# Kernel optimization log

Hardware: AMD Instinct MI355X
Metric: run time of the kernel (lower is better)

Reference implementation:

```python
import jax, jax.numpy as jnp
import numpy as np

B, L, D = 8, 1024, 768          # batch, seq_len, d_model
DI, DS, NL, DC = 1536, 16, 2, 4  # d_inner=2*d_model, d_state, n_layers, d_conv
DECAY, INSCALE = 0.9, 0.1
LN_EPS = 1e-5


def setup_inputs() -> dict:
    key = jax.random.key(0)
    ks = jax.random.split(key, 8)
    return {
        "x": jax.random.normal(ks[0], (B, L, D), jnp.float32),
        "in_proj_w": jax.random.normal(ks[1], (NL, D, 2 * DI), jnp.float32) * 0.02,
        "conv_w": jax.random.normal(ks[2], (NL, DI, DC), jnp.float32) * 0.1,
        "conv_b": jnp.zeros((NL, DI), jnp.float32),
        "out_proj_w": jax.random.normal(ks[3], (NL, DI, D), jnp.float32) * 0.02,
        "ln_gamma": jnp.ones((D,), jnp.float32),
        "ln_beta": jnp.zeros((D,), jnp.float32),
        # per-layer, per-timestep random state matrices (torch.randn inside the scan loop)
        "A": jax.random.normal(ks[4], (NL, L, DI, DS), jnp.float32),
        "Bm": jax.random.normal(ks[5], (NL, L, DS, DI), jnp.float32),
    }


def _silu(v):
    return v * jax.nn.sigmoid(v)


def _causal_dwconv(x, w, b):
    # x: [B, L, DI], w: [DI, DC], b: [DI]; torch Conv1d(groups=DI, padding=DC-1)[..., :L]
    xp = jnp.pad(x, ((0, 0), (DC - 1, 0), (0, 0)))
    out = b
    for k in range(DC):  # tiny fixed kernel loop
        out = out + w[:, k] * xp[:, k:k + L, :]
    return out


def _mamba_block(x, Wi, cw, cb, Wo, A_l, B_l):
    xz = jnp.einsum('bld,de->ble', x, Wi)
    x_in, z = jnp.split(xz, 2, axis=-1)          # each [B, L, DI]
    xc = _silu(_causal_dwconv(x_in, cw, cb))
    # selective scan: h_t = 0.9*h_{t-1} + 0.1 * x_t @ A_t ; y_t = h_t @ B_t
    u = INSCALE * jnp.einsum('blc,lcs->bls', xc, A_l)   # [B, L, DS]
    def step(h, u_t):
        h = DECAY * h + u_t
        return h, h
    _, hs = jax.lax.scan(step, jnp.zeros((x.shape[0], DS), x.dtype),
                         jnp.swapaxes(u, 0, 1))          # hs: [L, B, DS]
    x_ssm = jnp.einsum('lbs,lsc->blc', hs, B_l)          # [B, L, DI]
    y = x_ssm * _silu(z)
    return jnp.einsum('blc,cd->bld', y, Wo)


def reference(x, in_proj_w, conv_w, conv_b, out_proj_w, ln_gamma, ln_beta, A, Bm):
    for i in range(NL):  # residual fallback path of MambaSSM
        x = x + _mamba_block(x, in_proj_w[i], conv_w[i], conv_b[i],
                             out_proj_w[i], A[i], Bm[i])
    mu = jnp.mean(x, axis=-1, keepdims=True)
    var = jnp.mean(jnp.square(x - mu), axis=-1, keepdims=True)
    return (x - mu) / jnp.sqrt(var + LN_EPS) * ln_gamma + ln_beta
```

## Files before the change

kernel.cpp:

```cpp
#include <hip/hip_runtime.h>
#include <cstddef>
#include <cstdint>

constexpr int B  = 8;
constexpr int L  = 1024;
constexpr int D  = 768;
constexpr int DI = 1536;
constexpr int DS = 16;
constexpr int NL = 2;
constexpr float DECAY   = 0.9f;
constexpr float INSCALE = 0.1f;
constexpr float LN_EPS  = 1e-5f;

typedef __attribute__((ext_vector_type(8))) short bf16x8;
typedef __attribute__((ext_vector_type(4))) float f32x4;

typedef __attribute__((address_space(3))) uint32_t       lds_u32;
typedef const __attribute__((address_space(1))) uint32_t glb_u32;

__device__ __forceinline__ float siluf(float v) { return v / (1.0f + expf(-v)); }

__device__ __forceinline__ short f2bf(float f) {
  uint32_t u = __float_as_uint(f);
  u += 0x7fff + ((u >> 16) & 1);
  return (short)(u >> 16);
}
__device__ __forceinline__ float bf2f(short s) {
  return __uint_as_float(((uint32_t)(uint16_t)s) << 16);
}

__device__ __forceinline__ void load_lds16(const short* g, short* l) {
  __builtin_amdgcn_global_load_lds((glb_u32*)g, (lds_u32*)l, 16, 0, 0);
}

__device__ __forceinline__ int xcd_chunked(int lin, int nwg) {
  return (lin & 7) * (nwg >> 3) + (lin >> 3);
}

__global__ __launch_bounds__(256) void prep_kernel(const float* __restrict__ x,
                                                   float* __restrict__ xf,
                                                   short* __restrict__ xb,
                                                   const float* __restrict__ Wi,
                                                   const float* __restrict__ Wo,
                                                   short* __restrict__ Wt_i,
                                                   short* __restrict__ Wt_o) {
  int bid = blockIdx.x;
  if (bid < 6144) {
    int i = bid * 256 + threadIdx.x;
    float4 v = ((const float4*)x)[i];
    ((float4*)xf)[i] = v;
    short4 s;
    s.x = f2bf(v.x); s.y = f2bf(v.y); s.z = f2bf(v.z); s.w = f2bf(v.w);
    ((short4*)xb)[i] = s;
    return;
  }
  bid -= 6144;
  __shared__ float t[32][33];
  const int layer = bid / 3456;
  bid %= 3456;
  const float* W; short* Wt; int K, N, bx, by;
  if (bid < 2304) {
    W  = Wi  + (size_t)layer * D * 2 * DI;
    Wt = Wt_i + (size_t)layer * 2 * DI * D;
    K = D; N = 2 * DI; bx = bid % 96; by = bid / 96;
  } else {
    bid -= 2304;
    W  = Wo  + (size_t)layer * DI * D;
    Wt = Wt_o + (size_t)layer * D * DI;
    K = DI; N = D; bx = bid % 24; by = bid / 24;
  }
  const int n0 = bx * 32, k0 = by * 32;
  const int tx = threadIdx.x & 31, ty = threadIdx.x >> 5;
#pragma unroll
  for (int r = ty; r < 32; r += 8) t[r][tx] = W[(size_t)(k0 + r) * N + n0 + tx];
  __syncthreads();
#pragma unroll
  for (int r = ty; r < 32; r += 8) Wt[(size_t)(n0 + r) * K + k0 + tx] = f2bf(t[tx][r]);
}

template<int MODE>
__global__ __launch_bounds__(256) void gemm_bt(const short* __restrict__ A,
                                               const short* __restrict__ Bt,
                                               float* __restrict__ Pf,
                                               short* __restrict__ Pb,
                                               int M, int N, int K) {
  __shared__ short As[3][128 * 32];
  __shared__ short Bs[3][128 * 32];
  const int tid  = threadIdx.x;
  const int lane = tid & 63;
  const int w    = tid >> 6;
  const int wm   = w >> 1;
  const int wn   = w & 1;

  const int gx   = gridDim.x;
  const int lin  = blockIdx.y * gx + blockIdx.x;
  const int lgc  = xcd_chunked(lin, gx * gridDim.y);
  const int bn   = (lgc % gx) * 128;
  const int bm   = (lgc / gx) * 128;

  const int seg0 = w * 2;
  const int lane16 = lane << 4;
  const int P0 = (seg0 << 10) + lane16;
  const int Q0 = P0 ^ (((P0 >> 7) & 3) << 4);
  const int row0 = Q0 >> 6;
  const int g0   = (Q0 >> 4) & 3;
  const int P1 = ((seg0 + 1) << 10) + lane16;
  const int Q1 = P1 ^ (((P1 >> 7) & 3) << 4);
  const int row1 = Q1 >> 6;
  const int g1   = (Q1 >> 4) & 3;

  const short* gA0 = A  + (size_t)(bm + row0) * K + g0 * 8;
  const short* gA1 = A  + (size_t)(bm + row1) * K + g1 * 8;
  const short* gB0 = Bt + (size_t)(bn + row0) * K + g0 * 8;
  const short* gB1 = Bt + (size_t)(bn + row1) * K + g1 * 8;

  f32x4 acc[4][4];
#pragma unroll
  for (int i = 0; i < 4; ++i)
#pragma unroll
    for (int j = 0; j < 4; ++j) acc[i][j] = (f32x4)(0.f);

  const int fr = lane & 15;
  const int h8 = (lane >> 4) << 3;
  const int NT = K / 32;

  auto stage = [&](int bi, int k0) {
    load_lds16(gA0 + k0, &As[bi][(size_t)seg0 * 512]);
    load_lds16(gA1 + k0, &As[bi][(size_t)(seg0 + 1) * 512]);
    load_lds16(gB0 + k0, &Bs[bi][(size_t)seg0 * 512]);
    load_lds16(gB1 + k0, &Bs[bi][(size_t)(seg0 + 1) * 512]);
  };
  auto compute = [&](int bi) {
    bf16x8 af[4], bfr[4];
#pragma unroll
    for (int i = 0; i < 4; ++i) {
      const int r = wm * 64 + i * 16 + fr;
      int si = (r << 5) + h8;
      si ^= ((r >> 1) & 3) << 3;
      af[i] = *(const bf16x8*)&As[bi][si];
    }
#pragma unroll
    for (int j = 0; j < 4; ++j) {
      const int r = wn * 64 + j * 16 + fr;
      int si = (r << 5) + h8;
      si ^= ((r >> 1) & 3) << 3;
      bfr[j] = *(const bf16x8*)&Bs[bi][si];
    }
#pragma unroll
    for (int i = 0; i < 4; ++i)
#pragma unroll
      for (int j = 0; j < 4; ++j)
        acc[i][j] = __builtin_amdgcn_mfma_f32_16x16x32_bf16(af[i], bfr[j], acc[i][j], 0, 0, 0);
  };

  stage(0, 0);
  stage(1, 32);
  asm volatile("s_waitcnt vmcnt(4)" ::: "memory");
  asm volatile("s_barrier" ::: "memory");

  for (int t = 0; t < NT; t += 3) {
#pragma unroll
    for (int q = 0; q < 3; ++q) {
      const int tt = t + q;
      if (tt + 2 < NT) stage((q + 2) % 3, (tt + 2) * 32);
      compute(q);
      if (tt + 1 < NT) {
        if (tt + 2 < NT) asm volatile("s_waitcnt vmcnt(4)" ::: "memory");
        else             asm volatile("s_waitcnt vmcnt(0)" ::: "memory");
        asm volatile("s_barrier" ::: "memory");
      }
    }
  }

  const int orow = (lane >> 4) * 4;
  const int ocol = lane & 15;
#pragma unroll
  for (int i = 0; i < 4; ++i) {
#pragma unroll
    for (int r = 0; r < 4; ++r) {
      const size_t row = (size_t)(bm + wm * 64 + i * 16 + orow + r);
#pragma unroll
      for (int j = 0; j < 4; ++j) {
        const int col = bn + wn * 64 + j * 16 + ocol;
        float v = acc[i][j][r];
        if (MODE == 0) {
          if (col < DI) Pb[row * DI + col] = f2bf(v);
          else          Pb[(size_t)M * DI + row * DI + col - DI] = f2bf(v);
        } else {
          float o = Pf[row * N + col] + v;
          Pf[row * N + col] = o;
          Pb[row * N + col] = f2bf(o);
        }
      }
    }
  }
}

constexpr int CSL = DI / 4;
__global__ __launch_bounds__(256) void conv_u_kernel(const short* __restrict__ xin,
                                                     const float* __restrict__ cw,
                                                     const float* __restrict__ cb,
                                                     const float* __restrict__ A_l,
                                                     float* __restrict__ u_part) {
  const int lgc = xcd_chunked(blockIdx.x, L * 4);
  const int p = lgc & 3;
  const int l = lgc >> 2;
  const int c_base = p * CSL;
  __shared__ float xs[B][CSL];
  __shared__ float part[4][4][32];

  for (int i = threadIdx.x; i < B * (CSL / 4); i += 256) {
    const int b  = i / (CSL / 4);
    const int c4 = (i % (CSL / 4)) * 4;
    const int c  = c_base + c4;
    float4 q0 = *(const float4*)&cw[(c + 0) * 4];
    float4 q1 = *(const float4*)&cw[(c + 1) * 4];
    float4 q2 = *(const float4*)&cw[(c + 2) * 4];
    float4 q3 = *(const float4*)&cw[(c + 3) * 4];
    float4 acc = *(const float4*)&cb[c];
    const short* xp = xin + (size_t)b * L * DI + c;
#pragma unroll
    for (int k = 0; k < 4; ++k) {
      int lk = l - 3 + k;
      if (lk >= 0) {
        short4 xv = *(const short4*)&xp[(size_t)lk * DI];
        acc.x += (&q0.x)[k] * bf2f(xv.x);
        acc.y += (&q1.x)[k] * bf2f(xv.y);
        acc.z += (&q2.x)[k] * bf2f(xv.z);
        acc.w += (&q3.x)[k] * bf2f(xv.w);
      }
    }
    acc.x = siluf(acc.x); acc.y = siluf(acc.y);
    acc.z = siluf(acc.z); acc.w = siluf(acc.w);
    *(float4*)&xs[b][c4] = acc;
  }
  __syncthreads();

  const int s4 = threadIdx.x & 3;
  const int cg = threadIdx.x >> 2;
  const float* Ap = A_l + (size_t)l * DI * DS + s4 * 4;

  float4 acc[B];
#pragma unroll
  for (int b = 0; b < B; ++b) acc[b] = make_float4(0.f, 0.f, 0.f, 0.f);

#pragma unroll
  for (int c0 = 0; c0 < CSL; c0 += 64) {
    const int cl = c0 + cg;
    float4 a4 = *(const float4*)&Ap[(size_t)(c_base + cl) * DS];
#pragma unroll
    for (int b = 0; b < B; ++b) {
      float xv = xs[b][cl];
      acc[b].x += xv * a4.x; acc[b].y += xv * a4.y;
      acc[b].z += xv * a4.z; acc[b].w += xv * a4.w;
    }
  }

#pragma unroll
  for (int off = 32; off >= 4; off >>= 1) {
#pragma unroll
    for (int b = 0; b < B; ++b) {
      acc[b].x += __shfl_down(acc[b].x, off, 64);
      acc[b].y += __shfl_down(acc[b].y, off, 64);
      acc[b].z += __shfl_down(acc[b].z, off, 64);
      acc[b].w += __shfl_down(acc[b].w, off, 64);
    }
  }
  const int wv = threadIdx.x >> 6, lane = threadIdx.x & 63;
  if (lane < 4) {
#pragma unroll
    for (int b = 0; b < B; ++b) {
      part[wv][lane][b * 4 + 0] = acc[b].x;
      part[wv][lane][b * 4 + 1] = acc[b].y;
      part[wv][lane][b * 4 + 2] = acc[b].z;
      part[wv][lane][b * 4 + 3] = acc[b].w;
    }
  }
  __syncthreads();
  if (threadIdx.x < 128) {
    const int o  = threadIdx.x;
    const int b  = o >> 4;
    const int ss = (o >> 2) & 3;
    const int jj = o & 3;
    float s = part[0][ss][b * 4 + jj] + part[1][ss][b * 4 + jj] +
              part[2][ss][b * 4 + jj] + part[3][ss][b * 4 + jj];
    u_part[((size_t)l * 4 + p) * 128 + o] = INSCALE * s;
  }
}

__global__ __launch_bounds__(256) void scan_kernel(const float* __restrict__ u_part,
                                                   float* __restrict__ hs) {
  const int t = blockIdx.x;
  const int i = threadIdx.x;
  __shared__ float csc[256];

  float v[4];
#pragma unroll
  for (int j = 0; j < 4; ++j) {
    const float* up = u_part + ((size_t)(4 * i + j) * 4) * 128 + t;
    v[j] = (up[0] + up[128]) + (up[256] + up[384]);
  }
  const float p0 = v[0];
  const float p1 = p0 * DECAY + v[1];
  const float p2 = p1 * DECAY + v[2];
  const float p3 = p2 * DECAY + v[3];

  csc[i] = p3;
  __syncthreads();
  float f = DECAY * DECAY * DECAY * DECAY;
  for (int d = 1; d < 256; d <<= 1) {
    float add = (i >= d) ? csc[i - d] : 0.f;
    __syncthreads();
    csc[i] += add * f;
    __syncthreads();
    f *= f;
  }
  const float H = (i > 0) ? csc[i - 1] : 0.f;

  const float a1 = DECAY, a2 = DECAY * DECAY, a3 = a2 * DECAY, a4 = a2 * a2;
  float* hp = hs + (size_t)(4 * i) * 128 + t;
  hp[0]   = p0 + H * a1;
  hp[128] = p1 + H * a2;
  hp[256] = p2 + H * a3;
  hp[384] = p3 + H * a4;
}

__global__ __launch_bounds__(256) void xssm_kernel(const float* __restrict__ hs,
                                                   const float* __restrict__ B_l,
                                                   const short* __restrict__ zb,
                                                   short* __restrict__ y) {
  const int l0 = blockIdx.x * 2;
  const int cb = blockIdx.y * (DI / 3);
  __shared__ float hsl[2][128];
  const int t = threadIdx.x;
  hsl[t >> 7][t & 127] = hs[(size_t)(l0 + (t >> 7)) * 128 + (t & 127)];
  __syncthreads();

  const int li = t >> 7;
  const int l  = l0 + li;
  const int c  = cb + (t & 127) * 4;
  const float* Bp = B_l + (size_t)l * DS * DI + c;

  float4 acc[B];
#pragma unroll
  for (int b = 0; b < B; ++b) acc[b] = make_float4(0.f, 0.f, 0.f, 0.f);
#pragma unroll
  for (int s = 0; s < DS; ++s) {
    float4 bv = *(const float4*)&Bp[(size_t)s * DI];
#pragma unroll
    for (int b = 0; b < B; ++b) {
      float hv = hsl[li][b * DS + s];
      acc[b].x += hv * bv.x; acc[b].y += hv * bv.y;
      acc[b].z += hv * bv.z; acc[b].w += hv * bv.w;
    }
  }
#pragma unroll
  for (int b = 0; b < B; ++b) {
    short4 zs = *(const short4*)&zb[((size_t)b * L + l) * DI + c];
    short4 o;
    o.x = f2bf(acc[b].x * siluf(bf2f(zs.x)));
    o.y = f2bf(acc[b].y * siluf(bf2f(zs.y)));
    o.z = f2bf(acc[b].z * siluf(bf2f(zs.z)));
    o.w = f2bf(acc[b].w * siluf(bf2f(zs.w)));
    *(short4*)&y[((size_t)b * L + l) * DI + c] = o;
  }
}

__global__ __launch_bounds__(256) void ln_kernel(const float* __restrict__ x,
                                                 const float* __restrict__ gam,
                                                 const float* __restrict__ bet,
                                                 float* __restrict__ out) {
  const int row = blockIdx.x;
  const int t = threadIdx.x;
  const float* xr = x + (size_t)row * D;
  float v0 = xr[t], v1 = xr[t + 256], v2 = xr[t + 512];
  float s = v0 + v1 + v2;
  __shared__ float red[4], red2[4];
  const int wid = t >> 6, lane = t & 63;
#pragma unroll
  for (int off = 32; off > 0; off >>= 1) s += __shfl_down(s, off, 64);
  if (lane == 0) red[wid] = s;
  __syncthreads();
  float mu = (red[0] + red[1] + red[2] + red[3]) * (1.0f / D);
  float d0 = v0 - mu, d1 = v1 - mu, d2 = v2 - mu;
  float q = d0 * d0 + d1 * d1 + d2 * d2;
#pragma unroll
  for (int off = 32; off > 0; off >>= 1) q += __shfl_down(q, off, 64);
  if (lane == 0) red2[wid] = q;
  __syncthreads();
  float var = (red2[0] + red2[1] + red2[2] + red2[3]) * (1.0f / D);
  float rstd = rsqrtf(var + LN_EPS);
  size_t base = (size_t)row * D;
  out[base + t]       = d0 * rstd * gam[t]       + bet[t];
  out[base + t + 256] = d1 * rstd * gam[t + 256] + bet[t + 256];
  out[base + t + 512] = d2 * rstd * gam[t + 512] + bet[t + 512];
}

extern "C" void kernel_launch(void* const* d_in, const int* in_sizes, int n_in,
                              void* d_out, int out_size, void* d_ws, size_t ws_size,
                              hipStream_t stream) {
  (void)in_sizes; (void)n_in; (void)out_size; (void)ws_size;
  const float* x   = (const float*)d_in[0];
  const float* Wi  = (const float*)d_in[1];
  const float* cw  = (const float*)d_in[2];
  const float* cb  = (const float*)d_in[3];
  const float* Wo  = (const float*)d_in[4];
  const float* gam = (const float*)d_in[5];
  const float* bet = (const float*)d_in[6];
  const float* Am  = (const float*)d_in[7];
  const float* Bm  = (const float*)d_in[8];
  float* out = (float*)d_out;

  const size_t MN = (size_t)B * L;

  float* buf_x  = (float*)d_ws;
  short* buf_xb = (short*)(buf_x + MN * D);
  short* xin_b  = buf_xb + MN * D;
  short* zb     = xin_b + MN * DI;
  short* y_bf   = zb + MN * DI;
  float* u_part = (float*)(y_bf + MN * DI);
  float* buf_hs = u_part + (size_t)L * 4 * 128;
  short* Wt_i   = (short*)(buf_hs + (size_t)L * 128);
  short* Wt_o   = Wt_i + (size_t)NL * 2 * DI * D;

  prep_kernel<<<6144 + 3456 * NL, 256, 0, stream>>>(x, buf_x, buf_xb, Wi, Wo, Wt_i, Wt_o);

  for (int layer = 0; layer < NL; ++layer) {
    const float* cw_l = cw + (size_t)layer * DI * 4;
    const float* cb_l = cb + (size_t)layer * DI;
    const float* A_l  = Am + (size_t)layer * L * DI * DS;
    const float* B_l  = Bm + (size_t)layer * L * DS * DI;
    const short* Wti_l = Wt_i + (size_t)layer * 2 * DI * D;
    const short* Wto_l = Wt_o + (size_t)layer * D * DI;

    gemm_bt<0><<<dim3(2 * DI / 128, MN / 128), 256, 0, stream>>>(
        buf_xb, Wti_l, nullptr, xin_b, (int)MN, 2 * DI, D);

    conv_u_kernel<<<L * 4, 256, 0, stream>>>(xin_b, cw_l, cb_l, A_l, u_part);

    scan_kernel<<<128, 256, 0, stream>>>(u_part, buf_hs);

    xssm_kernel<<<dim3(L / 2, 3), 256, 0, stream>>>(buf_hs, B_l, zb, y_bf);

    gemm_bt<1><<<dim3(D / 128, MN / 128), 256, 0, stream>>>(
        y_bf, Wto_l, buf_x, buf_xb, (int)MN, D, DI);
  }

  ln_kernel<<<(int)MN, 256, 0, stream>>>(buf_x, gam, bet, out);
}
```

Baseline: 479.3 us.

## Split GEMM into specialized kernels with 64x128 out-proj tile, drop XCD remap

```diff
diff --git a/kernel.cpp b/kernel.cpp
--- a/kernel.cpp
+++ b/kernel.cpp
@@ -31,10 +31,6 @@
 
 __device__ __forceinline__ void load_lds16(const short* g, short* l) {
   __builtin_amdgcn_global_load_lds((glb_u32*)g, (lds_u32*)l, 16, 0, 0);
-}
-
-__device__ __forceinline__ int xcd_chunked(int lin, int nwg) {
-  return (lin & 7) * (nwg >> 3) + (lin >> 3);
 }
 
 __global__ __launch_bounds__(256) void prep_kernel(const float* __restrict__ x,
@@ -78,12 +74,10 @@
   for (int r = ty; r < 32; r += 8) Wt[(size_t)(n0 + r) * K + k0 + tx] = f2bf(t[tx][r]);
 }
 
-template<int MODE>
-__global__ __launch_bounds__(256) void gemm_bt(const short* __restrict__ A,
-                                               const short* __restrict__ Bt,
-                                               float* __restrict__ Pf,
-                                               short* __restrict__ Pb,
-                                               int M, int N, int K) {
+__global__ __launch_bounds__(256) void gemm_bt0(const short* __restrict__ A,
+                                                const short* __restrict__ Bt,
+                                                short* __restrict__ Pb,
+                                                int M, int N, int K) {
   __shared__ short As[3][128 * 32];
   __shared__ short Bs[3][128 * 32];
   const int tid  = threadIdx.x;
@@ -91,12 +85,8 @@
   const int w    = tid >> 6;
   const int wm   = w >> 1;
   const int wn   = w & 1;
-
-  const int gx   = gridDim.x;
-  const int lin  = blockIdx.y * gx + blockIdx.x;
-  const int lgc  = xcd_chunked(lin, gx * gridDim.y);
-  const int bn   = (lgc % gx) * 128;
-  const int bm   = (lgc / gx) * 128;
+  const int bm   = blockIdx.y * 128;
+  const int bn   = blockIdx.x * 128;
 
   const int seg0 = w * 2;
   const int lane16 = lane << 4;
@@ -183,14 +173,114 @@
       for (int j = 0; j < 4; ++j) {
         const int col = bn + wn * 64 + j * 16 + ocol;
         float v = acc[i][j][r];
-        if (MODE == 0) {
-          if (col < DI) Pb[row * DI + col] = f2bf(v);
-          else          Pb[(size_t)M * DI + row * DI + col - DI] = f2bf(v);
-        } else {
-          float o = Pf[row * N + col] + v;
-          Pf[row * N + col] = o;
-          Pb[row * N + col] = f2bf(o);
-        }
+        if (col < DI) Pb[row * DI + col] = f2bf(v);
+        else          Pb[(size_t)M * DI + row * DI + col - DI] = f2bf(v);
+      }
+    }
+  }
+}
+
+__global__ __launch_bounds__(256) void gemm_bt1(const short* __restrict__ A,
+                                                const short* __restrict__ Bt,
+                                                float* __restrict__ Pf,
+                                                short* __restrict__ Pb,
+                                                int M, int N, int K) {
+  __shared__ short As[3][64 * 32];
+  __shared__ short Bs[3][128 * 32];
+  const int tid  = threadIdx.x;
+  const int lane = tid & 63;
+  const int w    = tid >> 6;
+  const int bm   = blockIdx.y * 64;
+  const int bn   = blockIdx.x * 128;
+
+  const int lane16 = lane << 4;
+  const int PA = (w << 10) + lane16;
+  const int QA = PA ^ (((PA >> 7) & 3) << 4);
+  const int rowA = QA >> 6;
+  const int gA_  = (QA >> 4) & 3;
+  const int PB0 = ((2 * w) << 10) + lane16;
+  const int QB0 = PB0 ^ (((PB0 >> 7) & 3) << 4);
+  const int rowB0 = QB0 >> 6;
+  const int gB0_  = (QB0 >> 4) & 3;
+  const int PB1 = ((2 * w + 1) << 10) + lane16;
+  const int QB1 = PB1 ^ (((PB1 >> 7) & 3) << 4);
+  const int rowB1 = QB1 >> 6;
+  const int gB1_  = (QB1 >> 4) & 3;
+
+  const short* gA  = A  + (size_t)(bm + rowA) * K + gA_ * 8;
+  const short* gB0 = Bt + (size_t)(bn + rowB0) * K + gB0_ * 8;
+  const short* gB1 = Bt + (size_t)(bn + rowB1) * K + gB1_ * 8;
+
+  f32x4 acc[4][2];
+#pragma unroll
+  for (int i = 0; i < 4; ++i)
+#pragma unroll
+    for (int j = 0; j < 2; ++j) acc[i][j] = (f32x4)(0.f);
+
+  const int fr = lane & 15;
+  const int h8 = (lane >> 4) << 3;
+  const int NT = K / 32;
+
+  auto stage = [&](int bi, int k0) {
+    load_lds16(gA  + k0, &As[bi][(size_t)w * 512]);
+    load_lds16(gB0 + k0, &Bs[bi][(size_t)(2 * w) * 512]);
+    load_lds16(gB1 + k0, &Bs[bi][(size_t)(2 * w + 1) * 512]);
+  };
+  auto compute = [&](int bi) {
+    bf16x8 af[4], bfr[2];
+#pragma unroll
+    for (int i = 0; i < 4; ++i) {
+      const int r = i * 16 + fr;
+      int si = (r << 5) + h8;
+      si ^= ((r >> 1) & 3) << 3;
+      af[i] = *(const bf16x8*)&As[bi][si];
+    }
+#pragma unroll
+    for (int j = 0; j < 2; ++j) {
+      const int r = w * 32 + j * 16 + fr;
+      int si = (r << 5) + h8;
+      si ^= ((r >> 1) & 3) << 3;
+      bfr[j] = *(const bf16x8*)&Bs[bi][si];
+    }
+#pragma unroll
+    for (int i = 0; i < 4; ++i)
+#pragma unroll
+      for (int j = 0; j < 2; ++j)
+        acc[i][j] = __builtin_amdgcn_mfma_f32_16x16x32_bf16(af[i], bfr[j], acc[i][j], 0, 0, 0);
+  };
+
+  stage(0, 0);
+  stage(1, 32);
+  asm volatile("s_waitcnt vmcnt(3)" ::: "memory");
+  asm volatile("s_barrier" ::: "memory");
+
+  for (int t = 0; t < NT; t += 3) {
+#pragma unroll
+    for (int q = 0; q < 3; ++q) {
+      const int tt = t + q;
+      if (tt + 2 < NT) stage((q + 2) % 3, (tt + 2) * 32);
+      compute(q);
+      if (tt + 1 < NT) {
+        if (tt + 2 < NT) asm volatile("s_waitcnt vmcnt(3)" ::: "memory");
+        else             asm volatile("s_waitcnt vmcnt(0)" ::: "memory");
+        asm volatile("s_barrier" ::: "memory");
+      }
+    }
+  }
+
+  const int orow = (lane >> 4) * 4;
+  const int ocol = lane & 15;
+#pragma unroll
+  for (int i = 0; i < 4; ++i) {
+#pragma unroll
+    for (int r = 0; r < 4; ++r) {
+      const size_t row = (size_t)(bm + i * 16 + orow + r);
+#pragma unroll
+      for (int j = 0; j < 2; ++j) {
+        const int col = bn + w * 32 + j * 16 + ocol;
+        float o = Pf[row * N + col] + acc[i][j][r];
+        Pf[row * N + col] = o;
+        Pb[row * N + col] = f2bf(o);
       }
     }
   }
@@ -202,9 +292,8 @@
                                                      const float* __restrict__ cb,
                                                      const float* __restrict__ A_l,
                                                      float* __restrict__ u_part) {
-  const int lgc = xcd_chunked(blockIdx.x, L * 4);
-  const int p = lgc & 3;
-  const int l = lgc >> 2;
+  const int l = blockIdx.x;
+  const int p = blockIdx.y;
   const int c_base = p * CSL;
   __shared__ float xs[B][CSL];
   __shared__ float part[4][4][32];
@@ -433,16 +522,16 @@
     const short* Wti_l = Wt_i + (size_t)layer * 2 * DI * D;
     const short* Wto_l = Wt_o + (size_t)layer * D * DI;
 
-    gemm_bt<0><<<dim3(2 * DI / 128, MN / 128), 256, 0, stream>>>(
-        buf_xb, Wti_l, nullptr, xin_b, (int)MN, 2 * DI, D);
-
-    conv_u_kernel<<<L * 4, 256, 0, stream>>>(xin_b, cw_l, cb_l, A_l, u_part);
+    gemm_bt0<<<dim3(2 * DI / 128, MN / 128), 256, 0, stream>>>(
+        buf_xb, Wti_l, xin_b, (int)MN, 2 * DI, D);
+
+    conv_u_kernel<<<dim3(L, 4), 256, 0, stream>>>(xin_b, cw_l, cb_l, A_l, u_part);
 
     scan_kernel<<<128, 256, 0, stream>>>(u_part, buf_hs);
 
     xssm_kernel<<<dim3(L / 2, 3), 256, 0, stream>>>(buf_hs, B_l, zb, y_bf);
 
-    gemm_bt<1><<<dim3(D / 128, MN / 128), 256, 0, stream>>>(
+    gemm_bt1<<<dim3(D / 128, MN / 64), 256, 0, stream>>>(
         y_bf, Wto_l, buf_x, buf_xb, (int)MN, D, DI);
   }
 
```

Measured after the change: 457.5 us. -4.5%, faster.
